# Optimization experiments

Hardware: AMD Instinct MI355X
Metric: run time of the kernel (lower is better)

Reference implementation:

```python
import jax, jax.numpy as jnp
import numpy as np

IN_CH, OUT_CH, MODES1, MODES2 = 64, 64, 32, 32
B, H, W = 16, 256, 256


def setup_inputs() -> dict:
    key = jax.random.key(0)
    k = jax.random.split(key, 5)
    scale = (1.0 / (2 * IN_CH)) ** 0.5
    wshape = (IN_CH, OUT_CH, MODES1, MODES2)
    return {
        "x": jax.random.normal(k[0], (B, IN_CH, H, W), dtype=jnp.float32),
        "weights_pos_re": scale * jax.random.normal(k[1], wshape, dtype=jnp.float32),
        "weights_pos_im": scale * jax.random.normal(k[2], wshape, dtype=jnp.float32),
        "weights_neg_re": scale * jax.random.normal(k[3], wshape, dtype=jnp.float32),
        "weights_neg_im": scale * jax.random.normal(k[4], wshape, dtype=jnp.float32),
        "out_h": H,
        "out_w": W,
    }


def reference(x, weights_pos_re, weights_pos_im, weights_neg_re, weights_neg_im, out_h, out_w):
    b, c_in, in_h, in_w = x.shape
    wp = weights_pos_re + 1j * weights_pos_im  # complex64 [i, o, m1, m2]
    wn = weights_neg_re + 1j * weights_neg_im
    # rfft2 with norm='forward' divides by n (matches torch.fft.rfft2 norm='forward')
    x_ft = jnp.fft.rfft2(x, norm="forward")  # [b, i, in_h, in_w//2+1] complex64
    m1 = min(MODES1, in_h // 2, out_h // 2)
    m2 = min(MODES2, x_ft.shape[-1], out_w // 2 + 1)
    # truncated-mode complex channel mixing on low-frequency corners
    top = jnp.einsum("bixy,ioxy->boxy", x_ft[:, :, :m1, :m2], wp[:, :, :m1, :m2])
    bot = jnp.einsum("bixy,ioxy->boxy", x_ft[:, :, -m1:, :m2], wn[:, :, :m1, :m2])
    out_ft = jnp.zeros((b, OUT_CH, out_h, out_w // 2 + 1), dtype=jnp.complex64)
    out_ft = out_ft.at[:, :, :m1, :m2].set(top)
    out_ft = out_ft.at[:, :, -m1:, :m2].set(bot)
    # irfft2 with norm='forward' multiplies by n
    return jnp.fft.irfft2(out_ft, s=(out_h, out_w), norm="forward")
```

## Files before the change

### kernel.cpp

```cpp
#include <hip/hip_runtime.h>
#include <math.h>

#define PI_F 3.14159265358979323846f


static constexpr int T_FA  = 0;
static constexpr int T_FE  = 16384;
static constexpr int T_FBC = 32768;
static constexpr int T_FBS = 49152;
static constexpr int T_FD1 = 65536;
static constexpr int T_FD2 = 98304;
static constexpr int T_X2  = 131072;
static constexpr int T_CC  = 131072 + 4194304;

typedef __attribute__((ext_vector_type(8))) __bf16 bf16x8;
typedef __attribute__((ext_vector_type(4))) float f32x4;

union B4 { __bf16 b[4]; uint2 u; };

__global__ __launch_bounds__(256) void k_prep(float* __restrict__ ws) {
  int idx = blockIdx.x * 256 + threadIdx.x;
  const float C = 2.0f * PI_F / 256.0f;
  if (idx < 16384) {
    int j = idx;
    int e = j & 7, l = (j >> 3) & 63, q = j >> 9;
    int ns = q & 3, kc = q >> 2;
    int w = kc * 32 + ((l >> 4) & 3) * 8 + e;
    int col = ns * 16 + (l & 15);
    int kxi = col & 31;
    float ang = C * (float)((kxi * w) & 255);
    float v = (col < 32) ? cosf(ang) : -sinf(ang);
    __bf16 hv = (__bf16)v;
    __bf16 lv = (__bf16)(v - (float)hv);
    __bf16* fr = (__bf16*)(ws + T_FA);
    fr[j] = hv; fr[16384 + j] = lv;
  } else if (idx < 32768) {
    int j = idx - 16384;
    int e = j & 7, l = (j >> 3) & 63, q = j >> 9;
    int wb = q & 15, kc = q >> 4;
    int c = kc * 32 + ((l >> 4) & 3) * 8 + e;
    int w = wb * 16 + (l & 15);
    int kxi = (c < 32) ? c : (c - 32);
    float ang = C * (float)((kxi * w) & 255);
    float v = (c < 32) ? cosf(ang) : sinf(ang);
    __bf16 hv = (__bf16)v;
    __bf16 lv = (__bf16)(v - (float)hv);
    __bf16* fr = (__bf16*)(ws + T_FE);
    fr[j] = hv; fr[16384 + j] = lv;
  } else if (idx < 65536) {
    int base = (idx < 49152) ? 32768 : 49152;
    int j = idx - base;
    int e = j & 7, l = (j >> 3) & 63, q = j >> 9;
    int ms4 = q & 3, kc = q >> 2;
    int m = ms4 * 16 + (l & 15);
    int h = kc * 32 + ((l >> 4) & 3) * 8 + e;
    int ky = (m < 32) ? m : (m + 192);
    float ang = C * (float)((ky * h) & 255);
    float v = (idx < 49152) ? cosf(ang) : sinf(ang);
    __bf16 hv = (__bf16)v;
    __bf16 lv = (__bf16)(v - (float)hv);
    __bf16* fr = (__bf16*)(ws + base);
    fr[j] = hv; fr[16384 + j] = lv;
  } else if (idx < 131072) {
    int base = (idx < 98304) ? T_FD1 : T_FD2;
    int j = idx - base;
    int e = j & 7, l = (j >> 3) & 63, f = j >> 9;
    int nsH = f & 3, kc = (f >> 2) & 3, wv = f >> 4;
    int h = wv * 64 + nsH * 16 + (l & 15);
    int k = kc * 32 + ((l >> 4) & 3) * 8 + e;
    int m = (k < 64) ? k : (k - 64);
    int ky = (m < 32) ? m : (m + 192);
    float ang = C * (float)((ky * h) & 255);
    float cv = cosf(ang), sv = sinf(ang);
    float v;
    if (idx < 98304) v = (k < 64) ? cv : -sv;
    else             v = (k < 64) ? -sv : -cv;
    __bf16 hv = (__bf16)v;
    __bf16 lv = (__bf16)(v - (float)hv);
    __bf16* fr = (__bf16*)(ws + base);
    fr[j] = hv; fr[32768 + j] = lv;
  }
}

__device__ __forceinline__ void cvt_split8r(float4 a, float4 b,
                                            bf16x8& h, bf16x8& l) {
#define CVS(e, vv) { __bf16 hh = (__bf16)(vv); h[e] = hh; l[e] = (__bf16)((vv) - (float)hh); }
  CVS(0, a.x) CVS(1, a.y) CVS(2, a.z) CVS(3, a.w)
  CVS(4, b.x) CVS(5, b.y) CVS(6, b.z) CVS(7, b.w)
#undef CVS
}

__global__ __launch_bounds__(512, 2) void k_AB(const float* __restrict__ x,
                                               const float* __restrict__ ws,
                                               float2* __restrict__ X2) {
  __shared__ __bf16 AsH[16384];
  __shared__ __bf16 AsL[16384];
  const __bf16* frA = (const __bf16*)(ws + T_FA);
  const __bf16* fbc = (const __bf16*)(ws + T_FBC);
  const __bf16* fbs = (const __bf16*)(ws + T_FBS);
  const int t = threadIdx.x, bi = blockIdx.x;
  const int l = t & 63, wv = t >> 6;
  const int lr = l & 15, lk = l >> 4;

  f32x4 acc[2][4];
#pragma unroll
  for (int m = 0; m < 2; ++m)
#pragma unroll
    for (int n = 0; n < 4; ++n) acc[m][n] = (f32x4){0.f, 0.f, 0.f, 0.f};
  const float* xb = x + (size_t)bi * 65536 + (size_t)(wv * 32 + lr) * 256 + lk * 8;
  float4 xA[2], xB[2];
#pragma unroll
  for (int ms = 0; ms < 2; ++ms) {
    const float* p = xb + ms * 16 * 256;
    xA[ms] = *(const float4*)p;
    xB[ms] = *(const float4*)(p + 4);
  }
  for (int kc = 0; kc < 8; ++kc) {
    bf16x8 ah[2], al[2];
#pragma unroll
    for (int ms = 0; ms < 2; ++ms)
      cvt_split8r(xA[ms], xB[ms], ah[ms], al[ms]);
    if (kc < 7) {
#pragma unroll
      for (int ms = 0; ms < 2; ++ms) {
        const float* p = xb + ms * 16 * 256 + (kc + 1) * 32;
        xA[ms] = *(const float4*)p;
        xB[ms] = *(const float4*)(p + 4);
      }
    }
    bf16x8 bh[4], bl[4];
#pragma unroll
    for (int ns = 0; ns < 4; ++ns) {
      int fo = ((kc * 4 + ns) * 64 + l) * 8;
      bh[ns] = *(const bf16x8*)(frA + fo);
      bl[ns] = *(const bf16x8*)(frA + 16384 + fo);
    }
#pragma unroll
    for (int ms = 0; ms < 2; ++ms)
#pragma unroll
      for (int ns = 0; ns < 4; ++ns) {
        acc[ms][ns] = __builtin_amdgcn_mfma_f32_16x16x32_bf16(ah[ms], bh[ns], acc[ms][ns], 0, 0, 0);
        acc[ms][ns] = __builtin_amdgcn_mfma_f32_16x16x32_bf16(al[ms], bh[ns], acc[ms][ns], 0, 0, 0);
        acc[ms][ns] = __builtin_amdgcn_mfma_f32_16x16x32_bf16(ah[ms], bl[ns], acc[ms][ns], 0, 0, 0);
      }
  }
#pragma unroll
  for (int ms = 0; ms < 2; ++ms)
#pragma unroll
    for (int ns = 0; ns < 4; ++ns) {
      int lp = (ms * 2 + (lk >> 1)) * 16 + lr;
      int base = ((wv * 4 + ns) * 64 + lp) * 8 + (lk & 1) * 4;
      B4 ph, pl;
#pragma unroll
      for (int r = 0; r < 4; ++r) {
        float v = acc[ms][ns][r];
        __bf16 hv = (__bf16)v;
        ph.b[r] = hv; pl.b[r] = (__bf16)(v - (float)hv);
      }
      *(uint2*)&AsH[base] = ph.u;
      *(uint2*)&AsL[base] = pl.u;
    }
  __syncthreads();

  const int mS = wv & 3, nsP = wv >> 2;
  f32x4 cy0 = (f32x4){0.f,0.f,0.f,0.f}, cy1 = (f32x4){0.f,0.f,0.f,0.f};
  f32x4 sy0 = (f32x4){0.f,0.f,0.f,0.f}, sy1 = (f32x4){0.f,0.f,0.f,0.f};
  for (int kc = 0; kc < 8; ++kc) {
    int fo0 = ((kc * 4 + nsP) * 64 + l) * 8;
    int fo1 = ((kc * 4 + nsP + 2) * 64 + l) * 8;
    bf16x8 Bh0 = *(const bf16x8*)(AsH + fo0);
    bf16x8 Bl0 = *(const bf16x8*)(AsL + fo0);
    bf16x8 Bh1 = *(const bf16x8*)(AsH + fo1);
    bf16x8 Bl1 = *(const bf16x8*)(AsL + fo1);
    int ao = ((kc * 4 + mS) * 64 + l) * 8;
    bf16x8 cyh = *(const bf16x8*)(fbc + ao);
    bf16x8 cyl = *(const bf16x8*)(fbc + 16384 + ao);
    bf16x8 syh = *(const bf16x8*)(fbs + ao);
    bf16x8 syl = *(const bf16x8*)(fbs + 16384 + ao);
    cy0 = __builtin_amdgcn_mfma_f32_16x16x32_bf16(cyh, Bh0, cy0, 0, 0, 0);
    cy0 = __builtin_amdgcn_mfma_f32_16x16x32_bf16(cyl, Bh0, cy0, 0, 0, 0);
    cy0 = __builtin_amdgcn_mfma_f32_16x16x32_bf16(cyh, Bl0, cy0, 0, 0, 0);
    sy0 = __builtin_amdgcn_mfma_f32_16x16x32_bf16(syh, Bh0, sy0, 0, 0, 0);
    sy0 = __builtin_amdgcn_mfma_f32_16x16x32_bf16(syl, Bh0, sy0, 0, 0, 0);
    sy0 = __builtin_amdgcn_mfma_f32_16x16x32_bf16(syh, Bl0, sy0, 0, 0, 0);
    cy1 = __builtin_amdgcn_mfma_f32_16x16x32_bf16(cyh, Bh1, cy1, 0, 0, 0);
    cy1 = __builtin_amdgcn_mfma_f32_16x16x32_bf16(cyl, Bh1, cy1, 0, 0, 0);
    cy1 = __builtin_amdgcn_mfma_f32_16x16x32_bf16(cyh, Bl1, cy1, 0, 0, 0);
    sy1 = __builtin_amdgcn_mfma_f32_16x16x32_bf16(syh, Bh1, sy1, 0, 0, 0);
    sy1 = __builtin_amdgcn_mfma_f32_16x16x32_bf16(syl, Bh1, sy1, 0, 0, 0);
    sy1 = __builtin_amdgcn_mfma_f32_16x16x32_bf16(syh, Bl1, sy1, 0, 0, 0);
  }
#pragma unroll
  for (int r = 0; r < 4; ++r) {
    int m = mS * 16 + lk * 4 + r;
    int kx = nsP * 16 + lr;
    float re = cy0[r] + sy1[r];
    float im = cy1[r] - sy0[r];
    X2[(size_t)bi * 2048 + m * 32 + kx] = make_float2(re, im);
  }
}

__global__ __launch_bounds__(256, 4) void k_C(const float2* __restrict__ X2,
                                              const float* __restrict__ wpr,
                                              const float* __restrict__ wpi,
                                              const float* __restrict__ wnr,
                                              const float* __restrict__ wni,
                                              float2* __restrict__ Cc) {
  __shared__ float2 Xs[2][16][32];
  __shared__ float2 Ws[2][4][4][32];
  const int t = threadIdx.x;
  const int mc = blockIdx.x & 63, ot = blockIdx.x >> 6;
  const int mode0 = mc * 32;
  const float *wr, *wi; int wm0;
  if (mode0 < 1024) { wr = wpr; wi = wpi; wm0 = mode0; }
  else              { wr = wnr; wi = wni; wm0 = mode0 - 1024; }
  const int md = t & 31, og2 = (t >> 5) & 1, bq = t >> 6;
  const int bS = t >> 4, c2 = (t & 15) * 2;
  const int e0 = t * 2;
  const int wiS = e0 >> 7, wog = (e0 >> 5) & 3, wmd = e0 & 31;

  float ar[4][2], ai[4][2];
#pragma unroll
  for (int b = 0; b < 4; ++b) { ar[b][0]=0.f; ar[b][1]=0.f; ai[b][0]=0.f; ai[b][1]=0.f; }

  *(float4*)&Xs[0][bS][c2] =
      *(const float4*)&X2[((size_t)(bS * 64 + 0)) * 2048 + mode0 + c2];
  {
    size_t wa = ((size_t)(wiS * 64) + ot * 4 + wog) * 1024 + wm0 + wmd;
    float2 r2 = *(const float2*)&wr[wa];
    float2 i2 = *(const float2*)&wi[wa];
    Ws[0][wiS][wog][wmd]     = make_float2(r2.x, i2.x);
    Ws[0][wiS][wog][wmd + 1] = make_float2(r2.y, i2.y);
  }
  __syncthreads();

  for (int i = 0; i < 64; ++i) {
    const int cur = i & 1, wcur = (i >> 2) & 1;
    if (i < 63)
      *(float4*)&Xs[cur ^ 1][bS][c2] =
          *(const float4*)&X2[((size_t)(bS * 64 + i + 1)) * 2048 + mode0 + c2];
    if ((i & 3) == 0 && i < 60) {
      size_t wa = ((size_t)((i + 4 + wiS) * 64) + ot * 4 + wog) * 1024 + wm0 + wmd;
      float2 r2 = *(const float2*)&wr[wa];
      float2 i2 = *(const float2*)&wi[wa];
      Ws[wcur ^ 1][wiS][wog][wmd]     = make_float2(r2.x, i2.x);
      Ws[wcur ^ 1][wiS][wog][wmd + 1] = make_float2(r2.y, i2.y);
    }
    float2 w0 = Ws[wcur][i & 3][og2 * 2 + 0][md];
    float2 w1 = Ws[wcur][i & 3][og2 * 2 + 1][md];
#pragma unroll
    for (int b = 0; b < 4; ++b) {
      float2 xv = Xs[cur][bq * 4 + b][md];
      ar[b][0] = fmaf(xv.x, w0.x, fmaf(-xv.y, w0.y, ar[b][0]));
      ai[b][0] = fmaf(xv.x, w0.y, fmaf( xv.y, w0.x, ai[b][0]));
      ar[b][1] = fmaf(xv.x, w1.x, fmaf(-xv.y, w1.y, ar[b][1]));
      ai[b][1] = fmaf(xv.x, w1.y, fmaf( xv.y, w1.x, ai[b][1]));
    }
    __syncthreads();
  }

  const float scale = ((md == 0) ? 1.f : 2.f) * (1.f / 65536.f);
#pragma unroll
  for (int b = 0; b < 4; ++b)
#pragma unroll
    for (int o2 = 0; o2 < 2; ++o2)
      Cc[((size_t)((bq * 4 + b) * 64 + ot * 4 + og2 * 2 + o2)) * 2048 + mode0 + md] =
          make_float2(ar[b][o2] * scale, ai[b][o2] * scale);
}

__global__ __launch_bounds__(256, 2) void k_DE(const float2* __restrict__ Cc,
                                               const float* __restrict__ ws,
                                               float* __restrict__ out) {
  __shared__ __bf16 smem[16384];
  __bf16* CH = smem;
  __bf16* CL = smem + 4096;
  __bf16* EH = smem;
  __bf16* EL = smem + 8192;
  const __bf16* fd1 = (const __bf16*)(ws + T_FD1);
  const __bf16* fd2 = (const __bf16*)(ws + T_FD2);
  const __bf16* frE = (const __bf16*)(ws + T_FE);
  const int t = threadIdx.x, bo = blockIdx.x;
  const int l = t & 63, wv = t >> 6;
  const int lr = l & 15, lk = l >> 4;

  const float2* Cp = Cc + (size_t)bo * 2048;
#pragma unroll
  for (int jj = 0; jj < 8; ++jj) {
    int j = t + 256 * jj;
    float2 v = Cp[j];
    int m = j >> 5, kx = j & 31;
    int msK = kx >> 4, lA = ((m >> 3) & 3) * 16 + (kx & 15);
    int e = m & 7, kcR = m >> 5;
    int idxR = ((msK * 4 + kcR) * 64 + lA) * 8 + e;
    int idxI = ((msK * 4 + kcR + 2) * 64 + lA) * 8 + e;
    __bf16 h1 = (__bf16)v.x; CH[idxR] = h1; CL[idxR] = (__bf16)(v.x - (float)h1);
    __bf16 h2 = (__bf16)v.y; CH[idxI] = h2; CL[idxI] = (__bf16)(v.y - (float)h2);
  }
  __syncthreads();

  f32x4 z1[2][4], z2[2][4];
#pragma unroll
  for (int m = 0; m < 2; ++m)
#pragma unroll
    for (int n = 0; n < 4; ++n) { z1[m][n] = (f32x4){0.f,0.f,0.f,0.f}; z2[m][n] = (f32x4){0.f,0.f,0.f,0.f}; }
  for (int kc = 0; kc < 4; ++kc) {
    bf16x8 ah[2], al[2];
#pragma unroll
    for (int msK = 0; msK < 2; ++msK) {
      int fo = ((msK * 4 + kc) * 64 + l) * 8;
      ah[msK] = *(const bf16x8*)(CH + fo);
      al[msK] = *(const bf16x8*)(CL + fo);
    }
#pragma unroll
    for (int nsH = 0; nsH < 4; ++nsH) {
      int bo_ = (((wv * 4 + kc) * 4 + nsH) * 64 + l) * 8;
      bf16x8 b1h = *(const bf16x8*)(fd1 + bo_);
      bf16x8 b1l = *(const bf16x8*)(fd1 + 32768 + bo_);
      bf16x8 b2h = *(const bf16x8*)(fd2 + bo_);
      bf16x8 b2l = *(const bf16x8*)(fd2 + 32768 + bo_);
#pragma unroll
      for (int msK = 0; msK < 2; ++msK) {
        z1[msK][nsH] = __builtin_amdgcn_mfma_f32_16x16x32_bf16(ah[msK], b1h, z1[msK][nsH], 0, 0, 0);
        z1[msK][nsH] = __builtin_amdgcn_mfma_f32_16x16x32_bf16(al[msK], b1h, z1[msK][nsH], 0, 0, 0);
        z1[msK][nsH] = __builtin_amdgcn_mfma_f32_16x16x32_bf16(ah[msK], b1l, z1[msK][nsH], 0, 0, 0);
        z2[msK][nsH] = __builtin_amdgcn_mfma_f32_16x16x32_bf16(ah[msK], b2h, z2[msK][nsH], 0, 0, 0);
        z2[msK][nsH] = __builtin_amdgcn_mfma_f32_16x16x32_bf16(al[msK], b2h, z2[msK][nsH], 0, 0, 0);
        z2[msK][nsH] = __builtin_amdgcn_mfma_f32_16x16x32_bf16(ah[msK], b2l, z2[msK][nsH], 0, 0, 0);
      }
    }
  }
  __syncthreads();

  float* ob = out + (size_t)bo * 65536;
  for (int p = 0; p < 2; ++p) {
#pragma unroll
    for (int msK = 0; msK < 2; ++msK)
#pragma unroll
      for (int q = 0; q < 2; ++q) {
        int nsH = 2 * p + q;
        int lp = (msK * 2 + (lk >> 1)) * 16 + lr;
        int eb = (lk & 1) * 4;
        int base1 = (((wv * 2 + q) * 2 + 0) * 64 + lp) * 8 + eb;
        int base2 = (((wv * 2 + q) * 2 + 1) * 64 + lp) * 8 + eb;
        B4 p1h, p1l, p2h, p2l;
#pragma unroll
        for (int r = 0; r < 4; ++r) {
          float v1 = z1[msK][nsH][r];
          __bf16 h1 = (__bf16)v1; p1h.b[r] = h1; p1l.b[r] = (__bf16)(v1 - (float)h1);
          float v2 = z2[msK][nsH][r];
          __bf16 h2 = (__bf16)v2; p2h.b[r] = h2; p2l.b[r] = (__bf16)(v2 - (float)h2);
        }
        *(uint2*)&EH[base1] = p1h.u; *(uint2*)&EL[base1] = p1l.u;
        *(uint2*)&EH[base2] = p2h.u; *(uint2*)&EL[base2] = p2l.u;
      }
    bf16x8 ah[2][2], al[2][2];
#pragma unroll
    for (int q = 0; q < 2; ++q)
#pragma unroll
      for (int kc = 0; kc < 2; ++kc) {
        int fo = (((wv * 2 + q) * 2 + kc) * 64 + l) * 8;
        ah[q][kc] = *(const bf16x8*)(EH + fo);
        al[q][kc] = *(const bf16x8*)(EL + fo);
      }
    for (int cb = 0; cb < 4; ++cb) {
      f32x4 eacc[2][4];
#pragma unroll
      for (int m = 0; m < 2; ++m)
#pragma unroll
        for (int n = 0; n < 4; ++n) eacc[m][n] = (f32x4){0.f, 0.f, 0.f, 0.f};
#pragma unroll
      for (int kc = 0; kc < 2; ++kc) {
        bf16x8 bh[4], bl[4];
#pragma unroll
        for (int ns = 0; ns < 4; ++ns) {
          int fo = ((kc * 16 + cb * 4 + ns) * 64 + l) * 8;
          bh[ns] = *(const bf16x8*)(frE + fo);
          bl[ns] = *(const bf16x8*)(frE + 16384 + fo);
        }
#pragma unroll
        for (int q = 0; q < 2; ++q)
#pragma unroll
          for (int ns = 0; ns < 4; ++ns) {
            eacc[q][ns] = __builtin_amdgcn_mfma_f32_16x16x32_bf16(ah[q][kc], bh[ns], eacc[q][ns], 0, 0, 0);
            eacc[q][ns] = __builtin_amdgcn_mfma_f32_16x16x32_bf16(al[q][kc], bh[ns], eacc[q][ns], 0, 0, 0);
            eacc[q][ns] = __builtin_amdgcn_mfma_f32_16x16x32_bf16(ah[q][kc], bl[ns], eacc[q][ns], 0, 0, 0);
          }
      }
#pragma unroll
      for (int q = 0; q < 2; ++q)
#pragma unroll
        for (int ns = 0; ns < 4; ++ns) {
          int col = cb * 64 + ns * 16 + lr;
          int row0 = wv * 64 + (2 * p + q) * 16 + lk * 4;
#pragma unroll
          for (int r = 0; r < 4; ++r)
            ob[(size_t)(row0 + r) * 256 + col] = eacc[q][ns][r];
        }
    }
  }
}

extern "C" void kernel_launch(void* const* d_in, const int* in_sizes, int n_in,
                              void* d_out, int out_size, void* d_ws, size_t ws_size,
                              hipStream_t stream) {
  (void)in_sizes; (void)n_in; (void)out_size; (void)ws_size;
  const float* x   = (const float*)d_in[0];
  const float* wpr = (const float*)d_in[1];
  const float* wpi = (const float*)d_in[2];
  const float* wnr = (const float*)d_in[3];
  const float* wni = (const float*)d_in[4];
  float* out = (float*)d_out;
  float* ws  = (float*)d_ws;

  float2* X2 = (float2*)(ws + T_X2);
  float2* Cc = (float2*)(ws + T_CC);

  k_prep<<<512, 256, 0, stream>>>(ws);
  k_AB<<<1024, 512, 0, stream>>>(x, ws, X2);
  k_C<<<1024, 256, 0, stream>>>(X2, wpr, wpi, wnr, wni, Cc);
  k_DE<<<1024, 256, 0, stream>>>(Cc, ws, out);
}
```

Measured before the change: 215.8 us.

## Split k_DE work across 8 waves per block instead of 4

```diff
diff --git a/kernel.cpp b/kernel.cpp
--- a/kernel.cpp
+++ b/kernel.cpp
@@ -268,7 +268,7 @@
           make_float2(ar[b][o2] * scale, ai[b][o2] * scale);
 }
 
-__global__ __launch_bounds__(256, 2) void k_DE(const float2* __restrict__ Cc,
+__global__ __launch_bounds__(512, 2) void k_DE(const float2* __restrict__ Cc,
                                                const float* __restrict__ ws,
                                                float* __restrict__ out) {
   __shared__ __bf16 smem[16384];
@@ -280,13 +280,14 @@
   const __bf16* fd2 = (const __bf16*)(ws + T_FD2);
   const __bf16* frE = (const __bf16*)(ws + T_FE);
   const int t = threadIdx.x, bo = blockIdx.x;
-  const int l = t & 63, wv = t >> 6;
+  const int l = t & 63, wvp = t >> 6;
   const int lr = l & 15, lk = l >> 4;
+  const int wv = wvp >> 1, half = wvp & 1;
 
   const float2* Cp = Cc + (size_t)bo * 2048;
 #pragma unroll
-  for (int jj = 0; jj < 8; ++jj) {
-    int j = t + 256 * jj;
+  for (int jj = 0; jj < 4; ++jj) {
+    int j = t + 512 * jj;
     float2 v = Cp[j];
     int m = j >> 5, kx = j & 31;
     int msK = kx >> 4, lA = ((m >> 3) & 3) * 16 + (kx & 15);
@@ -298,11 +299,11 @@
   }
   __syncthreads();
 
-  f32x4 z1[2][4], z2[2][4];
+  f32x4 z1[2][2], z2[2][2];
 #pragma unroll
   for (int m = 0; m < 2; ++m)
 #pragma unroll
-    for (int n = 0; n < 4; ++n) { z1[m][n] = (f32x4){0.f,0.f,0.f,0.f}; z2[m][n] = (f32x4){0.f,0.f,0.f,0.f}; }
+    for (int n = 0; n < 2; ++n) { z1[m][n] = (f32x4){0.f,0.f,0.f,0.f}; z2[m][n] = (f32x4){0.f,0.f,0.f,0.f}; }
   for (int kc = 0; kc < 4; ++kc) {
     bf16x8 ah[2], al[2];
 #pragma unroll
@@ -312,7 +313,8 @@
       al[msK] = *(const bf16x8*)(CL + fo);
     }
 #pragma unroll
-    for (int nsH = 0; nsH < 4; ++nsH) {
+    for (int q = 0; q < 2; ++q) {
+      int nsH = half * 2 + q;
       int bo_ = (((wv * 4 + kc) * 4 + nsH) * 64 + l) * 8;
       bf16x8 b1h = *(const bf16x8*)(fd1 + bo_);
       bf16x8 b1l = *(const bf16x8*)(fd1 + 32768 + bo_);
@@ -320,12 +322,12 @@
       bf16x8 b2l = *(const bf16x8*)(fd2 + 32768 + bo_);
 #pragma unroll
       for (int msK = 0; msK < 2; ++msK) {
-        z1[msK][nsH] = __builtin_amdgcn_mfma_f32_16x16x32_bf16(ah[msK], b1h, z1[msK][nsH], 0, 0, 0);
-        z1[msK][nsH] = __builtin_amdgcn_mfma_f32_16x16x32_bf16(al[msK], b1h, z1[msK][nsH], 0, 0, 0);
-        z1[msK][nsH] = __builtin_amdgcn_mfma_f32_16x16x32_bf16(ah[msK], b1l, z1[msK][nsH], 0, 0, 0);
-        z2[msK][nsH] = __builtin_amdgcn_mfma_f32_16x16x32_bf16(ah[msK], b2h, z2[msK][nsH], 0, 0, 0);
-        z2[msK][nsH] = __builtin_amdgcn_mfma_f32_16x16x32_bf16(al[msK], b2h, z2[msK][nsH], 0, 0, 0);
-        z2[msK][nsH] = __builtin_amdgcn_mfma_f32_16x16x32_bf16(ah[msK], b2l, z2[msK][nsH], 0, 0, 0);
+        z1[msK][q] = __builtin_amdgcn_mfma_f32_16x16x32_bf16(ah[msK], b1h, z1[msK][q], 0, 0, 0);
+        z1[msK][q] = __builtin_amdgcn_mfma_f32_16x16x32_bf16(al[msK], b1h, z1[msK][q], 0, 0, 0);
+        z1[msK][q] = __builtin_amdgcn_mfma_f32_16x16x32_bf16(ah[msK], b1l, z1[msK][q], 0, 0, 0);
+        z2[msK][q] = __builtin_amdgcn_mfma_f32_16x16x32_bf16(ah[msK], b2h, z2[msK][q], 0, 0, 0);
+        z2[msK][q] = __builtin_amdgcn_mfma_f32_16x16x32_bf16(al[msK], b2h, z2[msK][q], 0, 0, 0);
+        z2[msK][q] = __builtin_amdgcn_mfma_f32_16x16x32_bf16(ah[msK], b2l, z2[msK][q], 0, 0, 0);
       }
     }
   }
@@ -334,40 +336,33 @@
   float* ob = out + (size_t)bo * 65536;
   for (int p = 0; p < 2; ++p) {
 #pragma unroll
-    for (int msK = 0; msK < 2; ++msK)
-#pragma unroll
-      for (int q = 0; q < 2; ++q) {
-        int nsH = 2 * p + q;
-        int lp = (msK * 2 + (lk >> 1)) * 16 + lr;
-        int eb = (lk & 1) * 4;
-        int base1 = (((wv * 2 + q) * 2 + 0) * 64 + lp) * 8 + eb;
-        int base2 = (((wv * 2 + q) * 2 + 1) * 64 + lp) * 8 + eb;
-        B4 p1h, p1l, p2h, p2l;
-#pragma unroll
-        for (int r = 0; r < 4; ++r) {
-          float v1 = z1[msK][nsH][r];
-          __bf16 h1 = (__bf16)v1; p1h.b[r] = h1; p1l.b[r] = (__bf16)(v1 - (float)h1);
-          float v2 = z2[msK][nsH][r];
-          __bf16 h2 = (__bf16)v2; p2h.b[r] = h2; p2l.b[r] = (__bf16)(v2 - (float)h2);
-        }
-        *(uint2*)&EH[base1] = p1h.u; *(uint2*)&EL[base1] = p1l.u;
-        *(uint2*)&EH[base2] = p2h.u; *(uint2*)&EL[base2] = p2l.u;
-      }
-    bf16x8 ah[2][2], al[2][2];
-#pragma unroll
-    for (int q = 0; q < 2; ++q)
-#pragma unroll
-      for (int kc = 0; kc < 2; ++kc) {
-        int fo = (((wv * 2 + q) * 2 + kc) * 64 + l) * 8;
-        ah[q][kc] = *(const bf16x8*)(EH + fo);
-        al[q][kc] = *(const bf16x8*)(EL + fo);
-      }
+    for (int msK = 0; msK < 2; ++msK) {
+      int lp = (msK * 2 + (lk >> 1)) * 16 + lr;
+      int eb = (lk & 1) * 4;
+      int base1 = ((wvp * 2 + 0) * 64 + lp) * 8 + eb;
+      int base2 = ((wvp * 2 + 1) * 64 + lp) * 8 + eb;
+      B4 p1h, p1l, p2h, p2l;
+#pragma unroll
+      for (int r = 0; r < 4; ++r) {
+        float v1 = z1[msK][p][r];
+        __bf16 h1 = (__bf16)v1; p1h.b[r] = h1; p1l.b[r] = (__bf16)(v1 - (float)h1);
+        float v2 = z2[msK][p][r];
+        __bf16 h2 = (__bf16)v2; p2h.b[r] = h2; p2l.b[r] = (__bf16)(v2 - (float)h2);
+      }
+      *(uint2*)&EH[base1] = p1h.u; *(uint2*)&EL[base1] = p1l.u;
+      *(uint2*)&EH[base2] = p2h.u; *(uint2*)&EL[base2] = p2l.u;
+    }
+    bf16x8 ah[2], al[2];
+#pragma unroll
+    for (int kc = 0; kc < 2; ++kc) {
+      int fo = ((wvp * 2 + kc) * 64 + l) * 8;
+      ah[kc] = *(const bf16x8*)(EH + fo);
+      al[kc] = *(const bf16x8*)(EL + fo);
+    }
     for (int cb = 0; cb < 4; ++cb) {
-      f32x4 eacc[2][4];
-#pragma unroll
-      for (int m = 0; m < 2; ++m)
-#pragma unroll
-        for (int n = 0; n < 4; ++n) eacc[m][n] = (f32x4){0.f, 0.f, 0.f, 0.f};
+      f32x4 eacc[4];
+#pragma unroll
+      for (int n = 0; n < 4; ++n) eacc[n] = (f32x4){0.f, 0.f, 0.f, 0.f};
 #pragma unroll
       for (int kc = 0; kc < 2; ++kc) {
         bf16x8 bh[4], bl[4];
@@ -378,24 +373,20 @@
           bl[ns] = *(const bf16x8*)(frE + 16384 + fo);
         }
 #pragma unroll
-        for (int q = 0; q < 2; ++q)
-#pragma unroll
-          for (int ns = 0; ns < 4; ++ns) {
-            eacc[q][ns] = __builtin_amdgcn_mfma_f32_16x16x32_bf16(ah[q][kc], bh[ns], eacc[q][ns], 0, 0, 0);
-            eacc[q][ns] = __builtin_amdgcn_mfma_f32_16x16x32_bf16(al[q][kc], bh[ns], eacc[q][ns], 0, 0, 0);
-            eacc[q][ns] = __builtin_amdgcn_mfma_f32_16x16x32_bf16(ah[q][kc], bl[ns], eacc[q][ns], 0, 0, 0);
-          }
-      }
-#pragma unroll
-      for (int q = 0; q < 2; ++q)
-#pragma unroll
         for (int ns = 0; ns < 4; ++ns) {
-          int col = cb * 64 + ns * 16 + lr;
-          int row0 = wv * 64 + (2 * p + q) * 16 + lk * 4;
-#pragma unroll
-          for (int r = 0; r < 4; ++r)
-            ob[(size_t)(row0 + r) * 256 + col] = eacc[q][ns][r];
+          eacc[ns] = __builtin_amdgcn_mfma_f32_16x16x32_bf16(ah[kc], bh[ns], eacc[ns], 0, 0, 0);
+          eacc[ns] = __builtin_amdgcn_mfma_f32_16x16x32_bf16(al[kc], bh[ns], eacc[ns], 0, 0, 0);
+          eacc[ns] = __builtin_amdgcn_mfma_f32_16x16x32_bf16(ah[kc], bl[ns], eacc[ns], 0, 0, 0);
         }
+      }
+#pragma unroll
+      for (int ns = 0; ns < 4; ++ns) {
+        int col = cb * 64 + ns * 16 + lr;
+        int row0 = (wvp * 2 + p) * 16 + lk * 4;
+#pragma unroll
+        for (int r = 0; r < 4; ++r)
+          ob[(size_t)(row0 + r) * 256 + col] = eacc[ns][r];
+      }
     }
   }
 }
@@ -418,5 +409,5 @@
   k_prep<<<512, 256, 0, stream>>>(ws);
   k_AB<<<1024, 512, 0, stream>>>(x, ws, X2);
   k_C<<<1024, 256, 0, stream>>>(X2, wpr, wpi, wnr, wni, Cc);
-  k_DE<<<1024, 256, 0, stream>>>(Cc, ws, out);
-}
+  k_DE<<<1024, 512, 0, stream>>>(Cc, ws, out);
+}
```

After: 218.8 us. About the same (+1.4%).
